# Kernel optimization log

Measured on AMD Instinct MI355X. Metric: run time of the kernel, lower is better.

Reference implementation:

```python
import jax, jax.numpy as jnp
import numpy as np

MODES1 = 16
MODES2 = 16
KX_SIGMA = 1.0
B, T, H, W, C = 4, 32, 128, 128, 1

KY_KERNEL = np.array([[0.01, 0.02, 0.04, 0.02, 0.01],
                      [0.02, 0.06, 0.09, 0.06, 0.02],
                      [0.04, 0.09, 0.16, 0.09, 0.04],
                      [0.02, 0.06, 0.09, 0.06, 0.02],
                      [0.01, 0.02, 0.04, 0.02, 0.01]], dtype=np.float32)


def _spectral_mix(x, w1, w2):
    # x: (B,T,H,W,C); w1,w2: complex (C,C,m1,m2). FFT-mode-truncated mixing.
    b, t, h, w, c = x.shape
    xc = jnp.transpose(x, (0, 1, 4, 2, 3))            # (B,T,C,H,W)
    x_ft = jnp.fft.rfft2(xc)                          # (B,T,C,H,W//2+1)
    wr = w // 2 + 1
    out_ft = jnp.zeros((b, t, c, h, wr), dtype=x_ft.dtype)
    top = jnp.einsum('btixy,ioxy->btoxy', x_ft[:, :, :, :MODES1, :MODES2], w1)
    bot = jnp.einsum('btixy,ioxy->btoxy', x_ft[:, :, :, h - MODES1:, :MODES2], w2)
    out_ft = out_ft.at[:, :, :, :MODES1, :MODES2].set(top)
    out_ft = out_ft.at[:, :, :, h - MODES1:, :MODES2].set(bot)
    out = jnp.fft.irfft2(out_ft, s=(h, w))            # (B,T,C,H,W)
    return jnp.transpose(out, (0, 1, 3, 4, 2))


def _restricted_spectral(x, scalar):
    # diagonal (identity * scalar) spectral weights == scale truncated modes
    b, t, h, w, c = x.shape
    xc = jnp.transpose(x, (0, 1, 4, 2, 3))
    x_ft = jnp.fft.rfft2(xc)
    wr = w // 2 + 1
    out_ft = jnp.zeros((b, t, c, h, wr), dtype=x_ft.dtype)
    out_ft = out_ft.at[:, :, :, :MODES1, :MODES2].set(x_ft[:, :, :, :MODES1, :MODES2] * scalar)
    out_ft = out_ft.at[:, :, :, h - MODES1:, :MODES2].set(x_ft[:, :, :, h - MODES1:, :MODES2] * scalar)
    out = jnp.fft.irfft2(out_ft, s=(h, w))
    return jnp.transpose(out, (0, 1, 3, 4, 2))


def _circular_conv(value, kernel):
    # value: (B,T,H,W,1), kernel: (kh,kw); circular-pad cross-correlation
    b, t, h, w, _ = value.shape
    kh, kw = kernel.shape
    x = value.reshape(b * t, 1, h, w)
    xp = jnp.pad(x, ((0, 0), (0, 0), (kh // 2, kh - kh // 2 - 1), (kw // 2, kw - kw // 2 - 1)), mode='wrap')
    out = jax.lax.conv_general_dilated(xp, kernel[None, None], (1, 1), 'VALID',
                                       dimension_numbers=('NCHW', 'OIHW', 'NCHW'))
    return out.reshape(b, t, h, w, 1)


def setup_inputs() -> dict:
    key = jax.random.key(0)
    ks = jax.random.split(key, 10)
    z = jax.random.normal(ks[0], (B, T, 2 * H, W, C), dtype=jnp.float32)
    scale = 1.0 / (C * C)  # torch: scale * torch.rand(cfloat) -> uniform real & imag
    u = lambda k: scale * jax.random.uniform(k, (C, C, MODES1, MODES2), dtype=jnp.float32)
    return {
        'z': z,
        'qw1r': u(ks[1]), 'qw1i': u(ks[2]), 'qw2r': u(ks[3]), 'qw2i': u(ks[4]),
        'kw1r': u(ks[5]), 'kw1i': u(ks[6]), 'kw2r': u(ks[7]), 'kw2i': u(ks[8]),
        'icl_scalar': jnp.float32(0.1),
        'ky_kernel': jnp.asarray(KY_KERNEL),
    }


def reference(z, qw1r, qw1i, qw2r, qw2i, kw1r, kw1i, kw2r, kw2i, icl_scalar, ky_kernel):
    b, t, full_h, w, c = z.shape
    h = full_h // 2
    x, y = z[:, :, :h], z[:, :, h:]
    query = _spectral_mix(x, qw1r + 1j * qw1i, qw2r + 1j * qw2i)
    keyt = _spectral_mix(x, kw1r + 1j * kw1i, kw2r + 1j * kw2i)
    value = _restricted_spectral(y, icl_scalar)
    # laplacian kernel attention scores
    q_ = query.reshape(b, t, -1)
    k_ = keyt.reshape(b, t, -1)
    diff = q_[:, :, None, :] - k_[:, None, :, :]        # (B,T,T,H*W*C)
    l2 = jnp.sqrt(jnp.sum(diff * diff, axis=-1) + 1e-8)
    kx = jnp.exp(-l2 / KX_SIGMA)                         # (B,T,T)
    # mask: M @ kx zeros out last query row
    mask = jnp.concatenate([jnp.ones((t - 1,), jnp.float32), jnp.zeros((1,), jnp.float32)])
    kx = kx * mask[None, :, None]
    vc = _circular_conv(value, ky_kernel)                # (B,T,H,W,1)
    attn_y = jnp.einsum('bthwc,btq->bqhwc', vc, kx)      # (B,T,H,W,1)
    output = jnp.concatenate([jnp.zeros_like(x), attn_y], axis=2)
    return output, kx
```

## Files before the change

kernel.cpp:

```cpp
#include <hip/hip_runtime.h>
#include <math.h>

#define FVC_OFF   0
#define PHIQ_OFF  131072
#define PHIK_OFF  262144
#define KX_OFF    393216
#define OUT_KX_OFF 4194304

#define TWOPI_128 0.049087385212340517f

__global__ __launch_bounds__(256) void dft_rows_kernel(
    const float* __restrict__ z, float* __restrict__ Gout)
{
    __shared__ float ct[128], st[128];
    __shared__ float rows[16 * 132];
    __shared__ float2 tile[16 * 17];

    const int tid = threadIdx.x;
    const int img = blockIdx.x >> 3;
    const int c0  = blockIdx.x & 7;
    const int bt  = img & 127;
    const int isY = img >> 7;

    if (tid < 128) {
        float s, c;
        sincosf((float)tid * TWOPI_128, &s, &c);
        ct[tid] = c; st[tid] = s;
    }
    const float* xim = z + (size_t)bt * 32768 + (size_t)isY * 16384 + (size_t)c0 * 2048;
    {
        int q0 = tid, q1 = tid + 256;
        float4 a = *(const float4*)(xim + (q0 >> 5) * 128 + (q0 & 31) * 4);
        float4 b = *(const float4*)(xim + (q1 >> 5) * 128 + (q1 & 31) * 4);
        *(float4*)(rows + (q0 >> 5) * 132 + (q0 & 31) * 4) = a;
        *(float4*)(rows + (q1 >> 5) * 132 + (q1 & 31) * 4) = b;
    }
    __syncthreads();

    const int v  = tid & 15;
    const int hl = tid >> 4;
    float sr0 = 0.f, si0 = 0.f, sr1 = 0.f, si1 = 0.f;
    float sr2 = 0.f, si2 = 0.f, sr3 = 0.f, si3 = 0.f;
    const float4* rp = (const float4*)(rows + hl * 132);
    #pragma unroll 8
    for (int m = 0; m < 32; ++m) {
        float4 x4 = rp[m];
        int k = (v * m * 4) & 127;
        float c = ct[k], s = st[k];
        sr0 = fmaf(x4.x, c, sr0); si0 = fmaf(x4.x, s, si0);
        sr1 = fmaf(x4.y, c, sr1); si1 = fmaf(x4.y, s, si1);
        sr2 = fmaf(x4.z, c, sr2); si2 = fmaf(x4.z, s, si2);
        sr3 = fmaf(x4.w, c, sr3); si3 = fmaf(x4.w, s, si3);
    }
    float c1 = ct[v], s1 = st[v];
    float c2 = ct[(2 * v) & 127], s2 = st[(2 * v) & 127];
    float c3 = ct[(3 * v) & 127], s3 = st[(3 * v) & 127];
    float gr = sr0 + sr1 * c1 - si1 * s1 + sr2 * c2 - si2 * s2 + sr3 * c3 - si3 * s3;
    float gi = -(si0 + sr1 * s1 + si1 * c1 + sr2 * s2 + si2 * c2 + sr3 * s3 + si3 * c3);

    tile[v * 17 + hl] = make_float2(gr, gi);
    __syncthreads();
    const int vw = tid >> 4, hw = tid & 15;
    float2 val = tile[vw * 17 + hw];
    *(float2*)(Gout + (size_t)img * 4096 + vw * 256 + (c0 * 16 + hw) * 2) = val;
}

__global__ __launch_bounds__(256) void modes_kernel(
    const float* __restrict__ Gglob,
    const float* __restrict__ qw1r, const float* __restrict__ qw1i,
    const float* __restrict__ qw2r, const float* __restrict__ qw2i,
    const float* __restrict__ kw1r, const float* __restrict__ kw1i,
    const float* __restrict__ kw2r, const float* __restrict__ kw2i,
    const float* __restrict__ icl,  const float* __restrict__ ker,
    float* __restrict__ ws)
{
    __shared__ float ct[128], st[128];
    __shared__ float Gbuf[16 * 260];
    __shared__ float f0r[64], f0i[64];

    const int tid = threadIdx.x;
    const int img = blockIdx.x;
    const int bt  = img & 127;
    const int isY = img >> 7;

    if (tid < 128) {
        float s, c;
        sincosf((float)tid * TWOPI_128, &s, &c);
        ct[tid] = c; st[tid] = s;
    }
    const float* gsrc = Gglob + (size_t)img * 4096;
    #pragma unroll
    for (int it = 0; it < 4; ++it) {
        int q = tid + it * 256;
        float4 val = *(const float4*)(gsrc + q * 4);
        *(float4*)(Gbuf + (q >> 6) * 260 + (q & 63) * 4) = val;
    }
    __syncthreads();

    const int v  = tid & 15;
    const int ui = tid >> 4;
    const int u1 = ui + 112;

    float s0r[4] = {0.f, 0.f, 0.f, 0.f}, s0i[4] = {0.f, 0.f, 0.f, 0.f};
    float s1r[4] = {0.f, 0.f, 0.f, 0.f}, s1i[4] = {0.f, 0.f, 0.f, 0.f};
    const float4* gp = (const float4*)(Gbuf + v * 260);
    #pragma unroll 8
    for (int m = 0; m < 32; ++m) {
        float4 ga = gp[2 * m];
        float4 gb = gp[2 * m + 1];
        int k0 = (ui * 4 * m) & 127;
        int k1 = (k0 + 64 * m) & 127;
        float c0 = ct[k0], s0 = st[k0];
        float c1 = ct[k1], s1v = st[k1];
        s0r[0] = fmaf(ga.x, c0, fmaf(ga.y,  s0, s0r[0]));
        s0i[0] = fmaf(ga.y, c0, fmaf(-ga.x, s0, s0i[0]));
        s0r[1] = fmaf(ga.z, c0, fmaf(ga.w,  s0, s0r[1]));
        s0i[1] = fmaf(ga.w, c0, fmaf(-ga.z, s0, s0i[1]));
        s0r[2] = fmaf(gb.x, c0, fmaf(gb.y,  s0, s0r[2]));
        s0i[2] = fmaf(gb.y, c0, fmaf(-gb.x, s0, s0i[2]));
        s0r[3] = fmaf(gb.z, c0, fmaf(gb.w,  s0, s0r[3]));
        s0i[3] = fmaf(gb.w, c0, fmaf(-gb.z, s0, s0i[3]));
        s1r[0] = fmaf(ga.x, c1, fmaf(ga.y,  s1v, s1r[0]));
        s1i[0] = fmaf(ga.y, c1, fmaf(-ga.x, s1v, s1i[0]));
        s1r[1] = fmaf(ga.z, c1, fmaf(ga.w,  s1v, s1r[1]));
        s1i[1] = fmaf(ga.w, c1, fmaf(-ga.z, s1v, s1i[1]));
        s1r[2] = fmaf(gb.x, c1, fmaf(gb.y,  s1v, s1r[2]));
        s1i[2] = fmaf(gb.y, c1, fmaf(-gb.x, s1v, s1i[2]));
        s1r[3] = fmaf(gb.z, c1, fmaf(gb.w,  s1v, s1r[3]));
        s1i[3] = fmaf(gb.w, c1, fmaf(-gb.z, s1v, s1i[3]));
    }
    float m0r = s0r[0], m0i = s0i[0], m1r = s1r[0], m1i = s1i[0];
    #pragma unroll
    for (int j = 1; j < 4; ++j) {
        int b0 = (ui * j) & 127;
        float cb = ct[b0], sb = st[b0];
        m0r += s0r[j] * cb + s0i[j] * sb;
        m0i += s0i[j] * cb - s0r[j] * sb;
        int b1 = (u1 * j) & 127;
        cb = ct[b1]; sb = st[b1];
        m1r += s1r[j] * cb + s1i[j] * sb;
        m1i += s1i[j] * cb - s1r[j] * sb;
    }

    const int mi = ui * 16 + v;

    if (!isY) {
        float a = qw1r[mi], bq = qw1i[mi];
        float fqr0 = m0r * a - m0i * bq;
        float fqi0 = m0r * bq + m0i * a;
        a = qw2r[mi]; bq = qw2i[mi];
        float fqr1 = m1r * a - m1i * bq;
        float fqi1 = m1r * bq + m1i * a;
        a = kw1r[mi]; bq = kw1i[mi];
        float fkr0 = m0r * a - m0i * bq;
        float fki0 = m0r * bq + m0i * a;
        a = kw2r[mi]; bq = kw2i[mi];
        float fkr1 = m1r * a - m1i * bq;
        float fki1 = m1r * bq + m1i * a;

        float* PQ = ws + PHIQ_OFF + (size_t)bt * 1024;
        float* PK = ws + PHIK_OFF + (size_t)bt * 1024;
        const float c2 = 0.011048543456039806f;
        if (v >= 1) {
            int b0 = ((v - 1) * 32 + ui) * 2;
            int b1 = ((v - 1) * 32 + ui + 16) * 2;
            PQ[b0] = c2 * fqr0; PQ[b0 + 1] = c2 * fqi0;
            PQ[b1] = c2 * fqr1; PQ[b1 + 1] = c2 * fqi1;
            PK[b0] = c2 * fkr0; PK[b0 + 1] = c2 * fki0;
            PK[b1] = c2 * fkr1; PK[b1 + 1] = c2 * fki1;
        } else {
            f0r[ui]      = fqr0; f0i[ui]      = fqi0;
            f0r[ui + 16] = fqr1; f0i[ui + 16] = fqi1;
            f0r[32 + ui] = fkr0; f0i[32 + ui] = fki0;
            f0r[48 + ui] = fkr1; f0i[48 + ui] = fki1;
        }
        __syncthreads();
        const float c1n = 0.0078125f;
        if (tid == 0) {
            PQ[960] = c1n * f0r[0];
            PK[960] = c1n * f0r[32];
        } else if (tid <= 15) {
            int u = tid;
            float hr = 0.5f * (f0r[u] + f0r[32 - u]);
            float hi = 0.5f * (f0i[u] - f0i[32 - u]);
            int o = 961 + (u - 1) * 2;
            PQ[o] = c2 * hr; PQ[o + 1] = c2 * hi;
            hr = 0.5f * (f0r[32 + u] + f0r[32 + (32 - u)]);
            hi = 0.5f * (f0i[32 + u] - f0i[32 + (32 - u)]);
            PK[o] = c2 * hr; PK[o + 1] = c2 * hi;
        } else if (tid == 16) {
            PQ[991] = c2 * 0.5f * f0r[16]; PQ[992] = -c2 * 0.5f * f0i[16];
            PK[991] = c2 * 0.5f * f0r[48]; PK[992] = -c2 * 0.5f * f0i[48];
        } else if (tid < 48) {
            PQ[993 + (tid - 17)] = 0.f;
            PK[993 + (tid - 17)] = 0.f;
        }
    } else {
        float s = icl[0];
        float khr0 = 0.f, khi0 = 0.f, khr1 = 0.f, khi1 = 0.f;
        #pragma unroll
        for (int a2 = 0; a2 < 5; ++a2) {
            #pragma unroll
            for (int c3 = 0; c3 < 5; ++c3) {
                float kv = ker[a2 * 5 + c3];
                int e0 = (ui * (a2 - 2) + v * (c3 - 2)) & 127;
                khr0 = fmaf(kv, ct[e0], khr0);
                khi0 = fmaf(kv, st[e0], khi0);
                int e1 = (u1 * (a2 - 2) + v * (c3 - 2)) & 127;
                khr1 = fmaf(kv, ct[e1], khr1);
                khi1 = fmaf(kv, st[e1], khi1);
            }
        }
        const int g0 = mi;
        const int g1 = (ui + 16) * 16 + v;
        float* FV = ws + FVC_OFF + (size_t)bt * 1024;
        FV[g0 * 2]     = s * (m0r * khr0 - m0i * khi0);
        FV[g0 * 2 + 1] = s * (m0r * khi0 + m0i * khr0);
        FV[g1 * 2]     = s * (m1r * khr1 - m1i * khi1);
        FV[g1 * 2 + 1] = s * (m1r * khi1 + m1i * khr1);
    }
}

__global__ __launch_bounds__(256) void dist_kernel(
    float* __restrict__ ws, float* __restrict__ out)
{
    __shared__ float lq[8 * 132];
    const int tid = threadIdx.x;
    const int b = blockIdx.x >> 5;
    const int i = blockIdx.x & 31;

    const float* phq = ws + PHIQ_OFF + (size_t)(b * 32 + i) * 1024;
    {
        float4 val = *(const float4*)(phq + tid * 4);
        *(float4*)(lq + (tid >> 5) * 132 + (tid & 31) * 4) = val;
    }
    __syncthreads();

    const int j = tid >> 3, seg = tid & 7;
    const float4* kp = (const float4*)(ws + PHIK_OFF + (size_t)(b * 32 + j) * 1024) + seg * 32;
    const float4* qp = (const float4*)(lq + seg * 132);
    float acc = 0.f;
    #pragma unroll 8
    for (int t = 0; t < 32; ++t) {
        float4 kv = kp[t], qv = qp[t];
        float d0 = qv.x - kv.x, d1 = qv.y - kv.y;
        float d2 = qv.z - kv.z, d3 = qv.w - kv.w;
        acc = fmaf(d0, d0, acc); acc = fmaf(d1, d1, acc);
        acc = fmaf(d2, d2, acc); acc = fmaf(d3, d3, acc);
    }
    acc += __shfl_xor(acc, 1);
    acc += __shfl_xor(acc, 2);
    acc += __shfl_xor(acc, 4);
    if (seg == 0) {
        float l2  = sqrtf(acc + 1e-8f);
        float kxv = (i == 31) ? 0.f : expf(-l2);
        int o = (b * 32 + i) * 32 + j;
        ws[KX_OFF + o]      = kxv;
        out[OUT_KX_OFF + o] = kxv;
    }
}

__global__ __launch_bounds__(256) void mix_inv_kernel(
    const float* __restrict__ ws, float* __restrict__ out)
{
    __shared__ float ct[128], st[128];
    __shared__ float fm[1024];
    __shared__ float Ar[64 * 17], Ai[64 * 17];
    __shared__ float kxs[32];

    const int tid  = threadIdx.x;
    const int b    = blockIdx.x >> 6;
    const int q    = (blockIdx.x >> 1) & 31;
    const int half = blockIdx.x & 1;

    if (tid < 128) {
        float s, c;
        sincosf((float)tid * TWOPI_128, &s, &c);
        ct[tid] = c; st[tid] = s;
    }
    if (tid < 32) kxs[tid] = ws[KX_OFF + (size_t)(b * 32 + tid) * 32 + q];
    __syncthreads();

    float4 acc = make_float4(0.f, 0.f, 0.f, 0.f);
    const float4* FV = (const float4*)(ws + FVC_OFF) + (size_t)b * 32 * 256;
    for (int i = 0; i < 31; ++i) {
        float kv = kxs[i];
        float4 f = FV[(size_t)i * 256 + tid];
        acc.x = fmaf(kv, f.x, acc.x);
        acc.y = fmaf(kv, f.y, acc.y);
        acc.z = fmaf(kv, f.z, acc.z);
        acc.w = fmaf(kv, f.w, acc.w);
    }
    ((float4*)fm)[tid] = acc;
    __syncthreads();

    {
        const int hl = tid >> 2;
        const int vb = (tid & 3) * 4;
        const int h  = half * 64 + hl;
        float ar[4] = {0.f, 0.f, 0.f, 0.f}, ai[4] = {0.f, 0.f, 0.f, 0.f};
        #pragma unroll 4
        for (int ui2 = 0; ui2 < 32; ++ui2) {
            int u = (ui2 < 16) ? ui2 : ui2 + 96;
            int k = (u * h) & 127;
            float cc = ct[k], ss = st[k];
            const float4* fp = (const float4*)(fm + (ui2 * 16 + vb) * 2);
            float4 f01 = fp[0], f23 = fp[1];
            ar[0] = fmaf(f01.x, cc, fmaf(-f01.y, ss, ar[0]));
            ai[0] = fmaf(f01.x, ss, fmaf( f01.y, cc, ai[0]));
            ar[1] = fmaf(f01.z, cc, fmaf(-f01.w, ss, ar[1]));
            ai[1] = fmaf(f01.z, ss, fmaf( f01.w, cc, ai[1]));
            ar[2] = fmaf(f23.x, cc, fmaf(-f23.y, ss, ar[2]));
            ai[2] = fmaf(f23.x, ss, fmaf( f23.y, cc, ai[2]));
            ar[3] = fmaf(f23.z, cc, fmaf(-f23.w, ss, ar[3]));
            ai[3] = fmaf(f23.z, ss, fmaf( f23.w, cc, ai[3]));
        }
        #pragma unroll
        for (int vv = 0; vv < 4; ++vv) {
            Ar[hl * 17 + vb + vv] = ar[vv];
            Ai[hl * 17 + vb + vv] = ai[vv];
        }
    }
    __syncthreads();

    const int w2   = tid & 127;
    const int hpar = tid >> 7;
    float cw[16], sw[16];
    #pragma unroll
    for (int v = 1; v < 16; ++v) {
        int k = (v * w2) & 127;
        cw[v] = ct[k]; sw[v] = st[k];
    }
    const size_t obase = (size_t)(b * 32 + q) * 32768;
    for (int it = 0; it < 32; ++it) {
        int l = it * 2 + hpar;
        int r = half * 64 + l;
        const float* arp = Ar + l * 17;
        const float* aip = Ai + l * 17;
        float accp = arp[0];
        #pragma unroll
        for (int v = 1; v < 16; ++v)
            accp += 2.f * (arp[v] * cw[v] - aip[v] * sw[v]);
        out[obase + (size_t)r * 128 + w2] = 0.f;
        out[obase + (size_t)(128 + r) * 128 + w2] = accp * 6.103515625e-05f;
    }
}

extern "C" void kernel_launch(void* const* d_in, const int* in_sizes, int n_in,
                              void* d_out, int out_size, void* d_ws, size_t ws_size,
                              hipStream_t stream)
{
    (void)in_sizes; (void)n_in; (void)out_size; (void)ws_size;
    const float* z    = (const float*)d_in[0];
    const float* qw1r = (const float*)d_in[1];
    const float* qw1i = (const float*)d_in[2];
    const float* qw2r = (const float*)d_in[3];
    const float* qw2i = (const float*)d_in[4];
    const float* kw1r = (const float*)d_in[5];
    const float* kw1i = (const float*)d_in[6];
    const float* kw2r = (const float*)d_in[7];
    const float* kw2i = (const float*)d_in[8];
    const float* icl  = (const float*)d_in[9];
    const float* ker  = (const float*)d_in[10];
    float* ws  = (float*)d_ws;
    float* out = (float*)d_out;

    hipLaunchKernelGGL(dft_rows_kernel, dim3(2048), dim3(256), 0, stream, z, out);
    hipLaunchKernelGGL(modes_kernel, dim3(256), dim3(256), 0, stream,
                       out, qw1r, qw1i, qw2r, qw2i, kw1r, kw1i, kw2r, kw2i,
                       icl, ker, ws);
    hipLaunchKernelGGL(dist_kernel, dim3(128), dim3(256), 0, stream, ws, out);
    hipLaunchKernelGGL(mix_inv_kernel, dim3(256), dim3(256), 0, stream, ws, out);
}
```

Before: 119.4 us.

## Fuse distance and inverse-mix kernels; split modes kernel across more blocks

The distance kernel is merged into the inverse-mix kernel, so each block recomputes its own column of kernel scores in shared memory. This removes one launch and the workspace round-trip for kx. The modes kernel now runs 1024 blocks of 128 threads, each handling four v columns, and the inverse kernel uses 512 blocks that each produce a quarter of the rows, both to raise parallelism on a 256-CU part. In exchange, every inverse block recomputes a 32-entry distance column, so that work is repeated four times per query and the PHI buffers are read repeatedly.

```diff
diff --git a/kernel.cpp b/kernel.cpp
--- a/kernel.cpp
+++ b/kernel.cpp
@@ -4,7 +4,6 @@
 #define FVC_OFF   0
 #define PHIQ_OFF  131072
 #define PHIK_OFF  262144
-#define KX_OFF    393216
 #define OUT_KX_OFF 4194304
 
 #define TWOPI_128 0.049087385212340517f
@@ -65,7 +64,7 @@
     *(float2*)(Gout + (size_t)img * 4096 + vw * 256 + (c0 * 16 + hw) * 2) = val;
 }
 
-__global__ __launch_bounds__(256) void modes_kernel(
+__global__ __launch_bounds__(128) void modes_kernel(
     const float* __restrict__ Gglob,
     const float* __restrict__ qw1r, const float* __restrict__ qw1i,
     const float* __restrict__ qw2r, const float* __restrict__ qw2i,
@@ -75,251 +74,207 @@
     float* __restrict__ ws)
 {
     __shared__ float ct[128], st[128];
-    __shared__ float Gbuf[16 * 260];
+    __shared__ float Gbuf[4 * 260];
     __shared__ float f0r[64], f0i[64];
 
     const int tid = threadIdx.x;
-    const int img = blockIdx.x;
+    const int img = blockIdx.x >> 2;
+    const int vg  = blockIdx.x & 3;
     const int bt  = img & 127;
     const int isY = img >> 7;
 
-    if (tid < 128) {
+    {
         float s, c;
         sincosf((float)tid * TWOPI_128, &s, &c);
         ct[tid] = c; st[tid] = s;
     }
-    const float* gsrc = Gglob + (size_t)img * 4096;
-    #pragma unroll
-    for (int it = 0; it < 4; ++it) {
-        int q = tid + it * 256;
-        float4 val = *(const float4*)(gsrc + q * 4);
-        *(float4*)(Gbuf + (q >> 6) * 260 + (q & 63) * 4) = val;
-    }
-    __syncthreads();
-
-    const int v  = tid & 15;
-    const int ui = tid >> 4;
-    const int u1 = ui + 112;
-
-    float s0r[4] = {0.f, 0.f, 0.f, 0.f}, s0i[4] = {0.f, 0.f, 0.f, 0.f};
-    float s1r[4] = {0.f, 0.f, 0.f, 0.f}, s1i[4] = {0.f, 0.f, 0.f, 0.f};
-    const float4* gp = (const float4*)(Gbuf + v * 260);
+    const float4* gsrc = (const float4*)(Gglob + (size_t)img * 4096 + (size_t)vg * 1024);
+    {
+        float4 a = gsrc[tid];
+        float4 b = gsrc[tid + 128];
+        *(float4*)(Gbuf + (tid >> 6) * 260 + (tid & 63) * 4) = a;
+        *(float4*)(Gbuf + ((tid >> 6) + 2) * 260 + (tid & 63) * 4) = b;
+    }
+    __syncthreads();
+
+    const int uu = tid & 31;
+    const int vl = tid >> 5;
+    const int v  = vg * 4 + vl;
+    const int u  = (uu < 16) ? uu : uu + 96;
+
+    float sr[4] = {0.f, 0.f, 0.f, 0.f}, si[4] = {0.f, 0.f, 0.f, 0.f};
+    const float4* gp = (const float4*)(Gbuf + vl * 260);
     #pragma unroll 8
     for (int m = 0; m < 32; ++m) {
         float4 ga = gp[2 * m];
         float4 gb = gp[2 * m + 1];
-        int k0 = (ui * 4 * m) & 127;
-        int k1 = (k0 + 64 * m) & 127;
+        int k0 = (u * 4 * m) & 127;
         float c0 = ct[k0], s0 = st[k0];
-        float c1 = ct[k1], s1v = st[k1];
-        s0r[0] = fmaf(ga.x, c0, fmaf(ga.y,  s0, s0r[0]));
-        s0i[0] = fmaf(ga.y, c0, fmaf(-ga.x, s0, s0i[0]));
-        s0r[1] = fmaf(ga.z, c0, fmaf(ga.w,  s0, s0r[1]));
-        s0i[1] = fmaf(ga.w, c0, fmaf(-ga.z, s0, s0i[1]));
-        s0r[2] = fmaf(gb.x, c0, fmaf(gb.y,  s0, s0r[2]));
-        s0i[2] = fmaf(gb.y, c0, fmaf(-gb.x, s0, s0i[2]));
-        s0r[3] = fmaf(gb.z, c0, fmaf(gb.w,  s0, s0r[3]));
-        s0i[3] = fmaf(gb.w, c0, fmaf(-gb.z, s0, s0i[3]));
-        s1r[0] = fmaf(ga.x, c1, fmaf(ga.y,  s1v, s1r[0]));
-        s1i[0] = fmaf(ga.y, c1, fmaf(-ga.x, s1v, s1i[0]));
-        s1r[1] = fmaf(ga.z, c1, fmaf(ga.w,  s1v, s1r[1]));
-        s1i[1] = fmaf(ga.w, c1, fmaf(-ga.z, s1v, s1i[1]));
-        s1r[2] = fmaf(gb.x, c1, fmaf(gb.y,  s1v, s1r[2]));
-        s1i[2] = fmaf(gb.y, c1, fmaf(-gb.x, s1v, s1i[2]));
-        s1r[3] = fmaf(gb.z, c1, fmaf(gb.w,  s1v, s1r[3]));
-        s1i[3] = fmaf(gb.w, c1, fmaf(-gb.z, s1v, s1i[3]));
-    }
-    float m0r = s0r[0], m0i = s0i[0], m1r = s1r[0], m1i = s1i[0];
+        sr[0] = fmaf(ga.x, c0, fmaf(ga.y,  s0, sr[0]));
+        si[0] = fmaf(ga.y, c0, fmaf(-ga.x, s0, si[0]));
+        sr[1] = fmaf(ga.z, c0, fmaf(ga.w,  s0, sr[1]));
+        si[1] = fmaf(ga.w, c0, fmaf(-ga.z, s0, si[1]));
+        sr[2] = fmaf(gb.x, c0, fmaf(gb.y,  s0, sr[2]));
+        si[2] = fmaf(gb.y, c0, fmaf(-gb.x, s0, si[2]));
+        sr[3] = fmaf(gb.z, c0, fmaf(gb.w,  s0, sr[3]));
+        si[3] = fmaf(gb.w, c0, fmaf(-gb.z, s0, si[3]));
+    }
+    float mr = sr[0], mi_ = si[0];
     #pragma unroll
     for (int j = 1; j < 4; ++j) {
-        int b0 = (ui * j) & 127;
-        float cb = ct[b0], sb = st[b0];
-        m0r += s0r[j] * cb + s0i[j] * sb;
-        m0i += s0i[j] * cb - s0r[j] * sb;
-        int b1 = (u1 * j) & 127;
-        cb = ct[b1]; sb = st[b1];
-        m1r += s1r[j] * cb + s1i[j] * sb;
-        m1i += s1i[j] * cb - s1r[j] * sb;
-    }
-
-    const int mi = ui * 16 + v;
+        int k = (u * j) & 127;
+        float cb = ct[k], sb = st[k];
+        mr  += sr[j] * cb + si[j] * sb;
+        mi_ += si[j] * cb - sr[j] * sb;
+    }
+
+    const int wi = (uu & 15) * 16 + v;
 
     if (!isY) {
-        float a = qw1r[mi], bq = qw1i[mi];
-        float fqr0 = m0r * a - m0i * bq;
-        float fqi0 = m0r * bq + m0i * a;
-        a = qw2r[mi]; bq = qw2i[mi];
-        float fqr1 = m1r * a - m1i * bq;
-        float fqi1 = m1r * bq + m1i * a;
-        a = kw1r[mi]; bq = kw1i[mi];
-        float fkr0 = m0r * a - m0i * bq;
-        float fki0 = m0r * bq + m0i * a;
-        a = kw2r[mi]; bq = kw2i[mi];
-        float fkr1 = m1r * a - m1i * bq;
-        float fki1 = m1r * bq + m1i * a;
+        float a, bi_;
+        if (uu < 16) { a = qw1r[wi]; bi_ = qw1i[wi]; }
+        else         { a = qw2r[wi]; bi_ = qw2i[wi]; }
+        float fqr = mr * a - mi_ * bi_;
+        float fqi = mr * bi_ + mi_ * a;
+        if (uu < 16) { a = kw1r[wi]; bi_ = kw1i[wi]; }
+        else         { a = kw2r[wi]; bi_ = kw2i[wi]; }
+        float fkr = mr * a - mi_ * bi_;
+        float fki = mr * bi_ + mi_ * a;
 
         float* PQ = ws + PHIQ_OFF + (size_t)bt * 1024;
         float* PK = ws + PHIK_OFF + (size_t)bt * 1024;
         const float c2 = 0.011048543456039806f;
         if (v >= 1) {
-            int b0 = ((v - 1) * 32 + ui) * 2;
-            int b1 = ((v - 1) * 32 + ui + 16) * 2;
-            PQ[b0] = c2 * fqr0; PQ[b0 + 1] = c2 * fqi0;
-            PQ[b1] = c2 * fqr1; PQ[b1 + 1] = c2 * fqi1;
-            PK[b0] = c2 * fkr0; PK[b0 + 1] = c2 * fki0;
-            PK[b1] = c2 * fkr1; PK[b1 + 1] = c2 * fki1;
+            int o = ((v - 1) * 32 + uu) * 2;
+            PQ[o] = c2 * fqr; PQ[o + 1] = c2 * fqi;
+            PK[o] = c2 * fkr; PK[o + 1] = c2 * fki;
         } else {
-            f0r[ui]      = fqr0; f0i[ui]      = fqi0;
-            f0r[ui + 16] = fqr1; f0i[ui + 16] = fqi1;
-            f0r[32 + ui] = fkr0; f0i[32 + ui] = fki0;
-            f0r[48 + ui] = fkr1; f0i[48 + ui] = fki1;
+            f0r[uu]      = fqr; f0i[uu]      = fqi;
+            f0r[32 + uu] = fkr; f0i[32 + uu] = fki;
         }
         __syncthreads();
-        const float c1n = 0.0078125f;
-        if (tid == 0) {
-            PQ[960] = c1n * f0r[0];
-            PK[960] = c1n * f0r[32];
-        } else if (tid <= 15) {
-            int u = tid;
-            float hr = 0.5f * (f0r[u] + f0r[32 - u]);
-            float hi = 0.5f * (f0i[u] - f0i[32 - u]);
-            int o = 961 + (u - 1) * 2;
-            PQ[o] = c2 * hr; PQ[o + 1] = c2 * hi;
-            hr = 0.5f * (f0r[32 + u] + f0r[32 + (32 - u)]);
-            hi = 0.5f * (f0i[32 + u] - f0i[32 + (32 - u)]);
-            PK[o] = c2 * hr; PK[o + 1] = c2 * hi;
-        } else if (tid == 16) {
-            PQ[991] = c2 * 0.5f * f0r[16]; PQ[992] = -c2 * 0.5f * f0i[16];
-            PK[991] = c2 * 0.5f * f0r[48]; PK[992] = -c2 * 0.5f * f0i[48];
-        } else if (tid < 48) {
-            PQ[993 + (tid - 17)] = 0.f;
-            PK[993 + (tid - 17)] = 0.f;
+        if (vg == 0) {
+            const float c1n = 0.0078125f;
+            if (tid == 0) {
+                PQ[960] = c1n * f0r[0];
+                PK[960] = c1n * f0r[32];
+            } else if (tid <= 15) {
+                int uf = tid;
+                float hr = 0.5f * (f0r[uf] + f0r[32 - uf]);
+                float hi = 0.5f * (f0i[uf] - f0i[32 - uf]);
+                int o = 961 + (uf - 1) * 2;
+                PQ[o] = c2 * hr; PQ[o + 1] = c2 * hi;
+                hr = 0.5f * (f0r[32 + uf] + f0r[32 + (32 - uf)]);
+                hi = 0.5f * (f0i[32 + uf] - f0i[32 + (32 - uf)]);
+                PK[o] = c2 * hr; PK[o + 1] = c2 * hi;
+            } else if (tid == 16) {
+                PQ[991] = c2 * 0.5f * f0r[16]; PQ[992] = -c2 * 0.5f * f0i[16];
+                PK[991] = c2 * 0.5f * f0r[48]; PK[992] = -c2 * 0.5f * f0i[48];
+            } else if (tid < 48) {
+                PQ[993 + (tid - 17)] = 0.f;
+                PK[993 + (tid - 17)] = 0.f;
+            }
         }
     } else {
         float s = icl[0];
-        float khr0 = 0.f, khi0 = 0.f, khr1 = 0.f, khi1 = 0.f;
+        float khr = 0.f, khi = 0.f;
         #pragma unroll
         for (int a2 = 0; a2 < 5; ++a2) {
             #pragma unroll
             for (int c3 = 0; c3 < 5; ++c3) {
                 float kv = ker[a2 * 5 + c3];
-                int e0 = (ui * (a2 - 2) + v * (c3 - 2)) & 127;
-                khr0 = fmaf(kv, ct[e0], khr0);
-                khi0 = fmaf(kv, st[e0], khi0);
-                int e1 = (u1 * (a2 - 2) + v * (c3 - 2)) & 127;
-                khr1 = fmaf(kv, ct[e1], khr1);
-                khi1 = fmaf(kv, st[e1], khi1);
+                int e = (u * (a2 - 2) + v * (c3 - 2)) & 127;
+                khr = fmaf(kv, ct[e], khr);
+                khi = fmaf(kv, st[e], khi);
             }
         }
-        const int g0 = mi;
-        const int g1 = (ui + 16) * 16 + v;
+        const int slot = uu * 16 + v;
         float* FV = ws + FVC_OFF + (size_t)bt * 1024;
-        FV[g0 * 2]     = s * (m0r * khr0 - m0i * khi0);
-        FV[g0 * 2 + 1] = s * (m0r * khi0 + m0i * khr0);
-        FV[g1 * 2]     = s * (m1r * khr1 - m1i * khi1);
-        FV[g1 * 2 + 1] = s * (m1r * khi1 + m1i * khr1);
+        FV[slot * 2]     = s * (mr * khr - mi_ * khi);
+        FV[slot * 2 + 1] = s * (mr * khi + mi_ * khr);
     }
 }
 
-__global__ __launch_bounds__(256) void dist_kernel(
-    float* __restrict__ ws, float* __restrict__ out)
-{
-    __shared__ float lq[8 * 132];
-    const int tid = threadIdx.x;
-    const int b = blockIdx.x >> 5;
-    const int i = blockIdx.x & 31;
-
-    const float* phq = ws + PHIQ_OFF + (size_t)(b * 32 + i) * 1024;
-    {
-        float4 val = *(const float4*)(phq + tid * 4);
-        *(float4*)(lq + (tid >> 5) * 132 + (tid & 31) * 4) = val;
-    }
-    __syncthreads();
-
-    const int j = tid >> 3, seg = tid & 7;
-    const float4* kp = (const float4*)(ws + PHIK_OFF + (size_t)(b * 32 + j) * 1024) + seg * 32;
-    const float4* qp = (const float4*)(lq + seg * 132);
-    float acc = 0.f;
-    #pragma unroll 8
-    for (int t = 0; t < 32; ++t) {
-        float4 kv = kp[t], qv = qp[t];
-        float d0 = qv.x - kv.x, d1 = qv.y - kv.y;
-        float d2 = qv.z - kv.z, d3 = qv.w - kv.w;
-        acc = fmaf(d0, d0, acc); acc = fmaf(d1, d1, acc);
-        acc = fmaf(d2, d2, acc); acc = fmaf(d3, d3, acc);
-    }
-    acc += __shfl_xor(acc, 1);
-    acc += __shfl_xor(acc, 2);
-    acc += __shfl_xor(acc, 4);
-    if (seg == 0) {
-        float l2  = sqrtf(acc + 1e-8f);
-        float kxv = (i == 31) ? 0.f : expf(-l2);
-        int o = (b * 32 + i) * 32 + j;
-        ws[KX_OFF + o]      = kxv;
-        out[OUT_KX_OFF + o] = kxv;
-    }
-}
-
-__global__ __launch_bounds__(256) void mix_inv_kernel(
+__global__ __launch_bounds__(256) void dist_mix_inv_kernel(
     const float* __restrict__ ws, float* __restrict__ out)
 {
     __shared__ float ct[128], st[128];
-    __shared__ float fm[1024];
-    __shared__ float Ar[64 * 17], Ai[64 * 17];
     __shared__ float kxs[32];
-
-    const int tid  = threadIdx.x;
-    const int b    = blockIdx.x >> 6;
-    const int q    = (blockIdx.x >> 1) & 31;
-    const int half = blockIdx.x & 1;
+    __shared__ float fmP[32 * 36];
+    __shared__ float Ar[32 * 17], Ai[32 * 17];
+
+    const int tid     = threadIdx.x;
+    const int b       = blockIdx.x >> 7;
+    const int rest    = blockIdx.x & 127;
+    const int q       = rest >> 2;
+    const int quarter = rest & 3;
 
     if (tid < 128) {
         float s, c;
         sincosf((float)tid * TWOPI_128, &s, &c);
         ct[tid] = c; st[tid] = s;
     }
-    if (tid < 32) kxs[tid] = ws[KX_OFF + (size_t)(b * 32 + tid) * 32 + q];
-    __syncthreads();
-
-    float4 acc = make_float4(0.f, 0.f, 0.f, 0.f);
-    const float4* FV = (const float4*)(ws + FVC_OFF) + (size_t)b * 32 * 256;
-    for (int i = 0; i < 31; ++i) {
-        float kv = kxs[i];
-        float4 f = FV[(size_t)i * 256 + tid];
-        acc.x = fmaf(kv, f.x, acc.x);
-        acc.y = fmaf(kv, f.y, acc.y);
-        acc.z = fmaf(kv, f.z, acc.z);
-        acc.w = fmaf(kv, f.w, acc.w);
-    }
-    ((float4*)fm)[tid] = acc;
-    __syncthreads();
-
-    {
-        const int hl = tid >> 2;
-        const int vb = (tid & 3) * 4;
-        const int h  = half * 64 + hl;
-        float ar[4] = {0.f, 0.f, 0.f, 0.f}, ai[4] = {0.f, 0.f, 0.f, 0.f};
+
+    {
+        const int t = tid >> 3, seg = tid & 7;
+        const float4* qp = (const float4*)(ws + PHIQ_OFF + (size_t)(b * 32 + t) * 1024) + seg * 32;
+        const float4* kp = (const float4*)(ws + PHIK_OFF + (size_t)(b * 32 + q) * 1024) + seg * 32;
+        float acc = 0.f;
+        #pragma unroll 8
+        for (int d = 0; d < 32; ++d) {
+            float4 qv = qp[d], kv = kp[d];
+            float d0 = qv.x - kv.x, d1 = qv.y - kv.y;
+            float d2 = qv.z - kv.z, d3 = qv.w - kv.w;
+            acc = fmaf(d0, d0, acc); acc = fmaf(d1, d1, acc);
+            acc = fmaf(d2, d2, acc); acc = fmaf(d3, d3, acc);
+        }
+        acc += __shfl_xor(acc, 1);
+        acc += __shfl_xor(acc, 2);
+        acc += __shfl_xor(acc, 4);
+        if (seg == 0) {
+            float l2  = sqrtf(acc + 1e-8f);
+            float kxv = (t == 31) ? 0.f : expf(-l2);
+            kxs[t] = kxv;
+            if (quarter == 0)
+                out[OUT_KX_OFF + (b * 32 + t) * 32 + q] = kxv;
+        }
+    }
+    __syncthreads();
+
+    {
+        float4 acc = make_float4(0.f, 0.f, 0.f, 0.f);
+        const float4* FV = (const float4*)(ws + FVC_OFF) + (size_t)b * 32 * 256;
+        for (int i = 0; i < 31; ++i) {
+            float kv = kxs[i];
+            float4 f = FV[(size_t)i * 256 + tid];
+            acc.x = fmaf(kv, f.x, acc.x);
+            acc.y = fmaf(kv, f.y, acc.y);
+            acc.z = fmaf(kv, f.z, acc.z);
+            acc.w = fmaf(kv, f.w, acc.w);
+        }
+        int s0 = tid * 2;
+        *(float4*)(fmP + (s0 >> 4) * 36 + (s0 & 15) * 2) = acc;
+    }
+    __syncthreads();
+
+    {
+        const int hl = tid >> 3;
+        const int v0 = (tid & 7) * 2;
+        const int h  = quarter * 32 + hl;
+        float ar0 = 0.f, ai0 = 0.f, ar1 = 0.f, ai1 = 0.f;
         #pragma unroll 4
         for (int ui2 = 0; ui2 < 32; ++ui2) {
             int u = (ui2 < 16) ? ui2 : ui2 + 96;
             int k = (u * h) & 127;
             float cc = ct[k], ss = st[k];
-            const float4* fp = (const float4*)(fm + (ui2 * 16 + vb) * 2);
-            float4 f01 = fp[0], f23 = fp[1];
-            ar[0] = fmaf(f01.x, cc, fmaf(-f01.y, ss, ar[0]));
-            ai[0] = fmaf(f01.x, ss, fmaf( f01.y, cc, ai[0]));
-            ar[1] = fmaf(f01.z, cc, fmaf(-f01.w, ss, ar[1]));
-            ai[1] = fmaf(f01.z, ss, fmaf( f01.w, cc, ai[1]));
-            ar[2] = fmaf(f23.x, cc, fmaf(-f23.y, ss, ar[2]));
-            ai[2] = fmaf(f23.x, ss, fmaf( f23.y, cc, ai[2]));
-            ar[3] = fmaf(f23.z, cc, fmaf(-f23.w, ss, ar[3]));
-            ai[3] = fmaf(f23.z, ss, fmaf( f23.w, cc, ai[3]));
-        }
-        #pragma unroll
-        for (int vv = 0; vv < 4; ++vv) {
-            Ar[hl * 17 + vb + vv] = ar[vv];
-            Ai[hl * 17 + vb + vv] = ai[vv];
-        }
+            float4 f = *(const float4*)(fmP + ui2 * 36 + v0 * 2);
+            ar0 = fmaf(f.x, cc, fmaf(-f.y, ss, ar0));
+            ai0 = fmaf(f.x, ss, fmaf( f.y, cc, ai0));
+            ar1 = fmaf(f.z, cc, fmaf(-f.w, ss, ar1));
+            ai1 = fmaf(f.z, ss, fmaf( f.w, cc, ai1));
+        }
+        Ar[hl * 17 + v0]     = ar0; Ai[hl * 17 + v0]     = ai0;
+        Ar[hl * 17 + v0 + 1] = ar1; Ai[hl * 17 + v0 + 1] = ai1;
     }
     __syncthreads();
 
@@ -332,9 +287,9 @@
         cw[v] = ct[k]; sw[v] = st[k];
     }
     const size_t obase = (size_t)(b * 32 + q) * 32768;
-    for (int it = 0; it < 32; ++it) {
+    for (int it = 0; it < 16; ++it) {
         int l = it * 2 + hpar;
-        int r = half * 64 + l;
+        int r = quarter * 32 + l;
         const float* arp = Ar + l * 17;
         const float* aip = Ai + l * 17;
         float accp = arp[0];
@@ -366,9 +321,8 @@
     float* out = (float*)d_out;
 
     hipLaunchKernelGGL(dft_rows_kernel, dim3(2048), dim3(256), 0, stream, z, out);
-    hipLaunchKernelGGL(modes_kernel, dim3(256), dim3(256), 0, stream,
+    hipLaunchKernelGGL(modes_kernel, dim3(1024), dim3(128), 0, stream,
                        out, qw1r, qw1i, qw2r, qw2i, kw1r, kw1i, kw2r, kw2i,
                        icl, ker, ws);
-    hipLaunchKernelGGL(dist_kernel, dim3(128), dim3(256), 0, stream, ws, out);
-    hipLaunchKernelGGL(mix_inv_kernel, dim3(256), dim3(256), 0, stream, ws, out);
+    hipLaunchKernelGGL(dist_mix_inv_kernel, dim3(512), dim3(256), 0, stream, ws, out);
 }
```

Result: slower. 123.7 us (+3.6%).
